# Kernel tuning notes

Measured on AMD Instinct MI355X. Metric: run time of the kernel, lower is better.

## Reference

```python
import jax, jax.numpy as jnp
import numpy as np

N, E, G = 50000, 800000, 64   # nodes, edges, graphs
F, H, O = 6, 256, 2           # in_dim, hidden_dim, out_dim
NE, K, L = 8, 2, 4            # n_experts, top_k, n_layers


def setup_inputs() -> dict:
    key = jax.random.key(0)
    ks = jax.random.split(key, 12)
    s = 0.05
    return {
        "x": jax.random.normal(ks[0], (N, F), jnp.float32),
        "edge_index": jax.random.randint(ks[1], (2, E), 0, N),
        "batch": jnp.sort(jax.random.randint(ks[2], (N,), 0, G)),
        "enc_W": jax.random.normal(ks[3], (F, H), jnp.float32) * s,
        "enc_b": jnp.zeros((H,), jnp.float32),
        "rtr_W1": jax.random.normal(ks[4], (H + 2, H), jnp.float32) * s,
        "rtr_b1": jnp.zeros((H,), jnp.float32),
        "rtr_W2": jax.random.normal(ks[5], (H, NE), jnp.float32) * s,
        "rtr_b2": jnp.zeros((NE,), jnp.float32),
        "hid_Wr": jax.random.normal(ks[6], (L - 1, NE, H, H), jnp.float32) * s,
        "hid_Wn": jax.random.normal(ks[7], (L - 1, NE, H, H), jnp.float32) * s,
        "hid_b": jnp.zeros((L - 1, NE, H), jnp.float32),
        "out_Wr": jax.random.normal(ks[8], (NE, H, O), jnp.float32) * s,
        "out_Wn": jax.random.normal(ks[9], (NE, H, O), jnp.float32) * s,
        "out_b": jnp.zeros((NE, O), jnp.float32),
    }


def reference(x, edge_index, batch, enc_W, enc_b, rtr_W1, rtr_b1, rtr_W2, rtr_b2,
              hid_Wr, hid_Wn, hid_b, out_Wr, out_Wn, out_b):
    src, dst = edge_index[0], edge_index[1]

    # SharedBusEncoder: Linear + ReLU
    h = jax.nn.relu(x @ enc_W + enc_b)  # [N, H]

    # graph_size_features: per-graph node/edge counts, log-scaled, per node
    ones_n = jnp.ones((N,), h.dtype)
    nodes_per_g = jax.ops.segment_sum(ones_n, batch, num_segments=G)
    edges_per_g = jax.ops.segment_sum(jnp.ones((E,), h.dtype), batch[src], num_segments=G)
    size_feat = jnp.stack([jnp.log(nodes_per_g + 1.0)[batch],
                           jnp.log(edges_per_g + 1.0)[batch]], axis=-1)  # [N, 2]

    # BaseRouter: 2-layer MLP -> logits [N, NE]
    r = jax.nn.relu(jnp.concatenate([h, size_feat], axis=-1) @ rtr_W1 + rtr_b1)
    logits = r @ rtr_W2 + rtr_b2

    # sparse_routing (eval mode): softmax over top-k logits, scattered to dense mask
    vals, idx = jax.lax.top_k(logits, K)  # [N, K]
    w = jax.nn.softmax(vals, axis=-1)
    sparse = jnp.zeros((N, NE), h.dtype).at[jnp.arange(N)[:, None], idx].set(w)

    # Dense all-expert GraphConv stacks, mask-sum combine
    def graph_conv(he, Wr, Wn, b):
        agg = jax.ops.segment_sum(he[src], dst, num_segments=N)  # sum-aggregate neighbors
        return he @ Wr + agg @ Wn + b

    out = jnp.zeros((N, O), h.dtype)
    for e in range(NE):
        he = h
        for l in range(L - 1):
            he = jax.nn.relu(graph_conv(he, hid_Wr[l, e], hid_Wn[l, e], hid_b[l, e]))
        ye = graph_conv(he, out_Wr[e], out_Wn[e], out_b[e])  # [N, O]
        out = out + ye * sparse[:, e:e + 1]
    return out
```

## Files before the change

### kernel.cpp

```cpp
#include <hip/hip_runtime.h>
#include <cstdint>

#define NN 50000
#define EE 800000
#define GG 64

typedef unsigned short u16;
typedef __attribute__((ext_vector_type(8))) short bf16x8;
typedef __attribute__((ext_vector_type(4))) float f32x4;

__device__ __forceinline__ float bf2f(u16 v) { return __uint_as_float(((unsigned)v) << 16); }
__device__ __forceinline__ u16 f2bf(float f) {
  unsigned u = __float_as_uint(f);
  return (u16)((u + 0x7fffu + ((u >> 16) & 1u)) >> 16);
}

__device__ __forceinline__ void gload_lds16(const void* g, void* l) {
  __builtin_amdgcn_global_load_lds(
      (const __attribute__((address_space(1))) void*)g,
      (__attribute__((address_space(3))) void*)l,
      16, 0, 0);
}

__global__ void k_sentinel(float* out) { out[threadIdx.x] = 1e12f; }

__global__ __launch_bounds__(256) void k_hist(const int* __restrict__ ei,
                                              int* __restrict__ deg,
                                              int* __restrict__ outdeg) {
  int i = blockIdx.x * 256 + threadIdx.x;
  if (i < EE) {
    atomicAdd(&outdeg[ei[i]], 1);
    atomicAdd(&deg[ei[EE + i]], 1);
  }
}

__global__ __launch_bounds__(256) void k_graph_feats(const int* __restrict__ batch,
                                                     const int* __restrict__ outdeg,
                                                     float* __restrict__ gf) {
  __shared__ int red[256];
  int g = blockIdx.x, tid = threadIdx.x;
  auto lb = [&](int v) {
    int lo = 0, hi = NN;
    while (lo < hi) { int m = (lo + hi) >> 1; if (batch[m] < v) lo = m + 1; else hi = m; }
    return lo;
  };
  int bs = lb(g), be = lb(g + 1);
  int s = 0;
  for (int i = bs + tid; i < be; i += 256) s += outdeg[i];
  red[tid] = s;
  __syncthreads();
  for (int off = 128; off > 0; off >>= 1) {
    if (tid < off) red[tid] += red[tid + off];
    __syncthreads();
  }
  if (tid == 0) {
    gf[g * 2] = logf((float)(be - bs) + 1.f);
    gf[g * 2 + 1] = logf((float)red[0] + 1.f);
  }
}

__global__ __launch_bounds__(256) void k_router(
    const float* __restrict__ x, const float* __restrict__ encW, const float* __restrict__ encb,
    const int* __restrict__ batch, const float* __restrict__ gf,
    const float* __restrict__ W1, const float* __restrict__ b1,
    const float* __restrict__ W2, const float* __restrict__ b2,
    float* __restrict__ sparse, u16* __restrict__ hb_out) {
  __shared__ __align__(16) float hs_t[258][8];
  __shared__ __align__(16) float rs_t[256][8];
  __shared__ float part2[4][64];
  __shared__ float xv[8][6];
  __shared__ float sf[8][2];
  __shared__ float lg[8][8];
  int tid = threadIdx.x;
  int nb = blockIdx.x * 8;
  if (tid < 48) {
    int r = tid / 6, k = tid % 6;
    xv[r][k] = x[(nb + r) * 6 + k];
  }
  if (tid >= 48 && tid < 56) {
    int r = tid - 48;
    int g = batch[nb + r];
    sf[r][0] = gf[g * 2];
    sf[r][1] = gf[g * 2 + 1];
  }
  __syncthreads();
  {
    float wcol[6];
#pragma unroll
    for (int k = 0; k < 6; ++k) wcol[k] = encW[k * 256 + tid];
    float bb = encb[tid];
#pragma unroll
    for (int r = 0; r < 8; ++r) {
      float s = bb;
#pragma unroll
      for (int k = 0; k < 6; ++k) s += xv[r][k] * wcol[k];
      float h = fmaxf(s, 0.f);
      hs_t[tid][r] = h;
      hb_out[(nb + r) * 256 + tid] = f2bf(h);
    }
  }
  if (tid < 16) {
    int r = tid >> 1, c = tid & 1;
    hs_t[256 + c][r] = sf[r][c];
  }
  __syncthreads();
  float acc[8];
  {
    float bb = b1[tid];
#pragma unroll
    for (int r = 0; r < 8; ++r) acc[r] = bb;
  }
  int k = 0;
#pragma unroll 4
  for (; k < 256; ++k) {
    float w = W1[k * 256 + tid];
    float4 ha = *(const float4*)&hs_t[k][0];
    float4 hb4 = *(const float4*)&hs_t[k][4];
    acc[0] += ha.x * w; acc[1] += ha.y * w; acc[2] += ha.z * w; acc[3] += ha.w * w;
    acc[4] += hb4.x * w; acc[5] += hb4.y * w; acc[6] += hb4.z * w; acc[7] += hb4.w * w;
  }
  for (; k < 258; ++k) {
    float w = W1[k * 256 + tid];
    float4 ha = *(const float4*)&hs_t[k][0];
    float4 hb4 = *(const float4*)&hs_t[k][4];
    acc[0] += ha.x * w; acc[1] += ha.y * w; acc[2] += ha.z * w; acc[3] += ha.w * w;
    acc[4] += hb4.x * w; acc[5] += hb4.y * w; acc[6] += hb4.z * w; acc[7] += hb4.w * w;
  }
#pragma unroll
  for (int r = 0; r < 8; ++r) rs_t[tid][r] = fmaxf(acc[r], 0.f);
  __syncthreads();
  {
    int pr = tid & 63, pt = tid >> 6;
    int r = pr >> 3, e = pr & 7;
    float s = 0.f;
    int kk0 = pt * 64;
#pragma unroll 4
    for (int kk = kk0; kk < kk0 + 64; ++kk) s += rs_t[kk][r] * W2[kk * 8 + e];
    part2[pt][pr] = s;
  }
  __syncthreads();
  if (tid < 64) {
    int r = tid >> 3, e = tid & 7;
    lg[r][e] = b2[e] + part2[0][tid] + part2[1][tid] + part2[2][tid] + part2[3][tid];
  }
  __syncthreads();
  if (tid < 8) {
    int node = nb + tid;
    {
      float v1 = lg[tid][0];
      int j1 = 0;
#pragma unroll
      for (int j = 1; j < 8; ++j) {
        float v = lg[tid][j];
        if (v > v1) { v1 = v; j1 = j; }
      }
      float v2 = -1e30f;
      int j2 = 0;
#pragma unroll
      for (int j = 0; j < 8; ++j) {
        if (j == j1) continue;
        float v = lg[tid][j];
        if (v > v2) { v2 = v; j2 = j; }
      }
      float ex = expf(v2 - v1);
      float wa = 1.f / (1.f + ex), wb = ex / (1.f + ex);
      float* sp = sparse + node * 8;
#pragma unroll
      for (int j = 0; j < 8; ++j) sp[j] = 0.f;
      sp[j1] = wa;
      sp[j2] = wb;
    }
  }
}

__global__ __launch_bounds__(1024) void k_scan(const int* __restrict__ deg,
                                               int* __restrict__ rowptr) {
  __shared__ int tmp[1024];
  __shared__ int carry;
  if (threadIdx.x == 0) { carry = 0; rowptr[0] = 0; }
  __syncthreads();
  for (int base = 0; base < NN; base += 1024) {
    int i = base + threadIdx.x;
    int v = (i < NN) ? deg[i] : 0;
    tmp[threadIdx.x] = v;
    __syncthreads();
    for (int off = 1; off < 1024; off <<= 1) {
      int t = (threadIdx.x >= off) ? tmp[threadIdx.x - off] : 0;
      __syncthreads();
      tmp[threadIdx.x] += t;
      __syncthreads();
    }
    if (i < NN) rowptr[i + 1] = carry + tmp[threadIdx.x];
    int last = tmp[1023];
    __syncthreads();
    if (threadIdx.x == 0) carry += last;
    __syncthreads();
  }
}

__global__ __launch_bounds__(256) void k_fill(const int* __restrict__ ei,
                                              const int* __restrict__ rowptr,
                                              int* __restrict__ cursor, int* __restrict__ csrc) {
  int i = blockIdx.x * 256 + threadIdx.x;
  if (i < EE) {
    int s = ei[i], d = ei[EE + i];
    int pos = atomicAdd(&cursor[d], 1);
    csrc[rowptr[d] + pos] = s;
  }
}

__global__ __launch_bounds__(256) void k_spmm256(
    const int* __restrict__ rowptr, const int* __restrict__ csrc,
    const u16* __restrict__ X, u16* __restrict__ Y) {
  int wave = threadIdx.x >> 6, lane = threadIdx.x & 63;
  int d = blockIdx.x * 4 + wave;
  if (d >= NN) return;
  int s0 = rowptr[d], s1 = rowptr[d + 1];
  int c4 = lane * 4;
  float a0 = 0.f, a1 = 0.f, a2 = 0.f, a3 = 0.f;
  int i = s0;
  for (; i + 4 <= s1; i += 4) {
    int sa = csrc[i], sb = csrc[i + 1], sc = csrc[i + 2], sd = csrc[i + 3];
    ushort4 va = *(const ushort4*)(X + sa * 256 + c4);
    ushort4 vb = *(const ushort4*)(X + sb * 256 + c4);
    ushort4 vc = *(const ushort4*)(X + sc * 256 + c4);
    ushort4 vd = *(const ushort4*)(X + sd * 256 + c4);
    a0 += bf2f(va.x) + bf2f(vb.x) + bf2f(vc.x) + bf2f(vd.x);
    a1 += bf2f(va.y) + bf2f(vb.y) + bf2f(vc.y) + bf2f(vd.y);
    a2 += bf2f(va.z) + bf2f(vb.z) + bf2f(vc.z) + bf2f(vd.z);
    a3 += bf2f(va.w) + bf2f(vb.w) + bf2f(vc.w) + bf2f(vd.w);
  }
  for (; i < s1; ++i) {
    int sa = csrc[i];
    ushort4 va = *(const ushort4*)(X + sa * 256 + c4);
    a0 += bf2f(va.x);
    a1 += bf2f(va.y);
    a2 += bf2f(va.z);
    a3 += bf2f(va.w);
  }
  ushort4 o;
  o.x = f2bf(a0); o.y = f2bf(a1); o.z = f2bf(a2); o.w = f2bf(a3);
  *(ushort4*)(Y + d * 256 + c4) = o;
}

__global__ __launch_bounds__(256) void k_spmm_intl(
    const int* __restrict__ rowptr, const int* __restrict__ csrc,
    const u16* __restrict__ X, u16* __restrict__ Y, int rs) {
  int d = blockIdx.x;
  int tid = threadIdx.x;
  if (tid * 4 >= rs) return;
  int s0 = rowptr[d], s1 = rowptr[d + 1];
  int c4 = tid * 4;
  float a0 = 0.f, a1 = 0.f, a2 = 0.f, a3 = 0.f;
  int i = s0;
  for (; i + 4 <= s1; i += 4) {
    int sa = csrc[i], sb = csrc[i + 1], sc = csrc[i + 2], sd = csrc[i + 3];
    ushort4 va = *(const ushort4*)(X + (size_t)sa * rs + c4);
    ushort4 vb = *(const ushort4*)(X + (size_t)sb * rs + c4);
    ushort4 vc = *(const ushort4*)(X + (size_t)sc * rs + c4);
    ushort4 vd = *(const ushort4*)(X + (size_t)sd * rs + c4);
    a0 += bf2f(va.x) + bf2f(vb.x) + bf2f(vc.x) + bf2f(vd.x);
    a1 += bf2f(va.y) + bf2f(vb.y) + bf2f(vc.y) + bf2f(vd.y);
    a2 += bf2f(va.z) + bf2f(vb.z) + bf2f(vc.z) + bf2f(vd.z);
    a3 += bf2f(va.w) + bf2f(vb.w) + bf2f(vc.w) + bf2f(vd.w);
  }
  for (; i < s1; ++i) {
    int sa = csrc[i];
    ushort4 va = *(const ushort4*)(X + (size_t)sa * rs + c4);
    a0 += bf2f(va.x);
    a1 += bf2f(va.y);
    a2 += bf2f(va.z);
    a3 += bf2f(va.w);
  }
  ushort4 o;
  o.x = f2bf(a0); o.y = f2bf(a1); o.z = f2bf(a2); o.w = f2bf(a3);
  *(ushort4*)(Y + (size_t)d * rs + c4) = o;
}

__global__ __launch_bounds__(256) void k_transpose2(const float* __restrict__ Wr,
                                                    const float* __restrict__ Wn,
                                                    u16* __restrict__ WrT,
                                                    u16* __restrict__ WnT) {
  int idx = blockIdx.x * 256 + threadIdx.x;
  if (idx >= 24 * 65536) return;
  int m = idx >> 16, rem = idx & 65535;
  int k = rem >> 8, j = rem & 255;
  int o = (m << 16) + (j << 8) + k;
  WrT[o] = f2bf(Wr[idx]);
  WnT[o] = f2bf(Wn[idx]);
}

__global__ __launch_bounds__(512) void k_gemm(
    const u16* __restrict__ X1b, size_t x1gs, int x1rs,
    const u16* __restrict__ X2b, size_t x2gs, int x2rs,
    const u16* __restrict__ W1tb, const u16* __restrict__ W2tb, size_t wst,
    const float* __restrict__ biasb, size_t bst,
    u16* __restrict__ Yb, size_t ygs, int yrs, int relu,
    const float* __restrict__ oWr, const float* __restrict__ oWn, int e0_base,
    float* __restrict__ Y4self, float* __restrict__ Y4nb, int do_out) {
  __shared__ __align__(16) char smem[49152];
  int g = blockIdx.y;
  const u16* X1 = X1b + (size_t)g * x1gs;
  const u16* X2 = X2b + (size_t)g * x2gs;
  const u16* W1t = W1tb + (size_t)g * wst;
  const u16* W2t = W2tb + (size_t)g * wst;
  const float* bias = biasb + (size_t)g * bst;
  u16* Y = Yb + (size_t)g * ygs;
  int tid = threadIdx.x;
  int wave = tid >> 6, lane = tid & 63;
  int l15 = lane & 15, l4 = lane >> 4;
  int m0 = blockIdx.x * 128;
  int wr = wave >> 2, wc = wave & 3;
  const f32x4 fz = {0.f, 0.f, 0.f, 0.f};
  f32x4 acc[4][4];
#pragma unroll
  for (int a = 0; a < 4; ++a)
#pragma unroll
    for (int b = 0; b < 4; ++b) acc[a][b] = fz;

  auto stage = [&](int t) {
    const u16* xs = (t < 8) ? X1 : X2;
    int xrs = (t < 8) ? x1rs : x2rs;
    const u16* wsrc = (t < 8) ? W1t : W2t;
    int kb = (t & 7) * 32;
    int half = t & 1;
    {
      int flat = wave * 1024 + lane * 16;
      int row = flat >> 6, colb = flat & 63;
      int scol = colb ^ (((row >> 1) & 3) << 4);
      int gr = m0 + row;
      if (gr > NN - 1) gr = NN - 1;
      gload_lds16(xs + (size_t)gr * xrs + kb + (scol >> 1), smem + half * 8192 + flat);
    }
#pragma unroll
    for (int q = 0; q < 2; ++q) {
      int flat = q * 8192 + wave * 1024 + lane * 16;
      int row = flat >> 6, colb = flat & 63;
      int scol = colb ^ (((row >> 1) & 3) << 4);
      gload_lds16(wsrc + row * 256 + kb + (scol >> 1), smem + 16384 + half * 16384 + flat);
    }
  };

  stage(0);
  for (int kt = 0; kt < 16; ++kt) {
    if (kt < 15) {
      stage(kt + 1);
      asm volatile("s_waitcnt vmcnt(3)" ::: "memory");
    } else {
      asm volatile("s_waitcnt vmcnt(0)" ::: "memory");
    }
    __builtin_amdgcn_sched_barrier(0);
    __builtin_amdgcn_s_barrier();
    __builtin_amdgcn_sched_barrier(0);
    const char* Ab = smem + (kt & 1) * 8192;
    const char* Bb = smem + 16384 + (kt & 1) * 16384;
    bf16x8 af[4], bfv[4];
#pragma unroll
    for (int mi = 0; mi < 4; ++mi) {
      int r = wr * 64 + mi * 16 + l15;
      af[mi] = *(const bf16x8*)(Ab + r * 64 + ((l4 * 16) ^ (((r >> 1) & 3) << 4)));
    }
#pragma unroll
    for (int nj = 0; nj < 4; ++nj) {
      int c = wc * 64 + nj * 16 + l15;
      bfv[nj] = *(const bf16x8*)(Bb + c * 64 + ((l4 * 16) ^ (((c >> 1) & 3) << 4)));
    }
#pragma unroll
    for (int mi = 0; mi < 4; ++mi)
#pragma unroll
      for (int nj = 0; nj < 4; ++nj)
        acc[mi][nj] =
            __builtin_amdgcn_mfma_f32_16x16x32_bf16(af[mi], bfv[nj], acc[mi][nj], 0, 0, 0);
    __builtin_amdgcn_sched_barrier(0);
    __builtin_amdgcn_s_barrier();
  }

  if (!do_out) {
#pragma unroll
    for (int mi = 0; mi < 4; ++mi) {
      int rbase = m0 + wr * 64 + mi * 16 + l4 * 4;
#pragma unroll
      for (int nj = 0; nj < 4; ++nj) {
        int col = wc * 64 + nj * 16 + l15;
        float bv = bias[col];
#pragma unroll
        for (int r2 = 0; r2 < 4; ++r2) {
          int row = rbase + r2;
          if (row < NN) {
            float v = acc[mi][nj][r2] + bv;
            if (relu) v = fmaxf(v, 0.f);
            Y[(size_t)row * yrs + col] = f2bf(v);
          }
        }
      }
    }
  } else {
    int eabs = e0_base + g;
    const float2* wr2p = (const float2*)(oWr + (size_t)eabs * 512);
    const float2* wn2p = (const float2*)(oWn + (size_t)eabs * 512);
    float bv[4]; float2 wa[4], wb[4];
#pragma unroll
    for (int nj = 0; nj < 4; ++nj) {
      int col = wc * 64 + nj * 16 + l15;
      bv[nj] = bias[col];
      wa[nj] = wr2p[col];
      wb[nj] = wn2p[col];
    }
    float* y4red = (float*)smem;
#pragma unroll
    for (int mi = 0; mi < 4; ++mi) {
#pragma unroll
      for (int r2 = 0; r2 < 4; ++r2) {
        float p0 = 0.f, p1 = 0.f, p2 = 0.f, p3 = 0.f;
#pragma unroll
        for (int nj = 0; nj < 4; ++nj) {
          float v = fmaxf(acc[mi][nj][r2] + bv[nj], 0.f);
          p0 += v * wa[nj].x; p1 += v * wa[nj].y;
          p2 += v * wb[nj].x; p3 += v * wb[nj].y;
        }
#pragma unroll
        for (int off2 = 1; off2 < 16; off2 <<= 1) {
          p0 += __shfl_xor(p0, off2); p1 += __shfl_xor(p1, off2);
          p2 += __shfl_xor(p2, off2); p3 += __shfl_xor(p3, off2);
        }
        if (l15 == 0) {
          int lr = wr * 64 + mi * 16 + l4 * 4 + r2;
          float* q = y4red + (lr * 4 + wc) * 4;
          q[0] = p0; q[1] = p1; q[2] = p2; q[3] = p3;
        }
      }
    }
    __syncthreads();
    if (tid < 128) {
      int row = m0 + tid;
      if (row < NN) {
        float s0 = 0.f, s1 = 0.f, n0 = 0.f, n1 = 0.f;
#pragma unroll
        for (int w2 = 0; w2 < 4; ++w2) {
          const float* q = y4red + (tid * 4 + w2) * 4;
          s0 += q[0]; s1 += q[1]; n0 += q[2]; n1 += q[3];
        }
        Y4self[row * 16 + eabs * 2] = s0;
        Y4self[row * 16 + eabs * 2 + 1] = s1;
        Y4nb[row * 16 + eabs * 2] = n0;
        Y4nb[row * 16 + eabs * 2 + 1] = n1;
      }
    }
  }
}

__global__ __launch_bounds__(256) void k_combine(
    const int* __restrict__ rowptr, const int* __restrict__ csrc,
    const float* __restrict__ Y4self, const float* __restrict__ Y4nb,
    const float* __restrict__ sparse, const float* __restrict__ ob,
    float* __restrict__ out) {
  int t = blockIdx.x * 256 + threadIdx.x;
  int d = t >> 3, e = t & 7;
  if (d >= NN) return;
  float s0 = Y4self[d * 16 + e * 2], s1 = Y4self[d * 16 + e * 2 + 1];
  float n0 = 0.f, n1 = 0.f;
  for (int i = rowptr[d]; i < rowptr[d + 1]; ++i) {
    int s = csrc[i];
    float2 v = *(const float2*)(Y4nb + s * 16 + e * 2);
    n0 += v.x;
    n1 += v.y;
  }
  float w = sparse[d * 8 + e];
  float t0 = w * (s0 + n0 + ob[e * 2]);
  float t1 = w * (s1 + n1 + ob[e * 2 + 1]);
  t0 += __shfl_xor(t0, 1); t1 += __shfl_xor(t1, 1);
  t0 += __shfl_xor(t0, 2); t1 += __shfl_xor(t1, 2);
  t0 += __shfl_xor(t0, 4); t1 += __shfl_xor(t1, 4);
  if (e == 0) {
    out[d * 2] = t0;
    out[d * 2 + 1] = t1;
  }
}

extern "C" void kernel_launch(void* const* d_in, const int* in_sizes, int n_in,
                              void* d_out, int out_size, void* d_ws, size_t ws_size,
                              hipStream_t stream) {
  const float* x = (const float*)d_in[0];
  const int* ei = (const int*)d_in[1];
  const int* batch = (const int*)d_in[2];
  const float* enc_W = (const float*)d_in[3];
  const float* enc_b = (const float*)d_in[4];
  const float* rW1 = (const float*)d_in[5];
  const float* rb1 = (const float*)d_in[6];
  const float* rW2 = (const float*)d_in[7];
  const float* rb2 = (const float*)d_in[8];
  const float* hid_Wr = (const float*)d_in[9];
  const float* hid_Wn = (const float*)d_in[10];
  const float* hid_b = (const float*)d_in[11];
  const float* out_Wr = (const float*)d_in[12];
  const float* out_Wn = (const float*)d_in[13];
  const float* out_b = (const float*)d_in[14];
  float* out = (float*)d_out;

  char* ws = (char*)d_ws;
  size_t off = 0;
  auto alloc = [&](size_t bytes) -> void* {
    void* p = ws + off;
    off = (off + bytes + 511) & ~(size_t)511;
    return p;
  };
  const size_t HBYTES = (size_t)NN * 256 * 2;
  u16* hb = (u16*)alloc(HBYTES);
  u16* agg0 = (u16*)alloc(HBYTES);
  u16* WrT = (u16*)alloc((size_t)24 * 65536 * 2);
  u16* WnT = (u16*)alloc((size_t)24 * 65536 * 2);
  int* deg = (int*)alloc((size_t)NN * 4);
  int* cursor = (int*)alloc((size_t)NN * 4);
  int* outdeg = (int*)alloc((size_t)NN * 4);
  size_t zero_bytes = (size_t)((char*)(outdeg + NN) - (char*)deg);
  int* rowptr = (int*)alloc((size_t)(NN + 1) * 4);
  int* csrc = (int*)alloc((size_t)EE * 4);
  float* gf = (float*)alloc(GG * 2 * 4);
  float* sparse = (float*)alloc((size_t)NN * 8 * 4);
  float* Y4self = (float*)alloc((size_t)NN * 16 * 4);
  float* Y4nb = (float*)alloc((size_t)NN * 16 * 4);

  size_t rem = (ws_size > off) ? ws_size - off : 0;
  size_t per = 2 * HBYTES + 2048;
  int grp = (rem >= 4 * per) ? 4 : (rem >= 2 * per) ? 2 : (rem >= per) ? 1 : 0;
  if (grp == 0) {
    k_sentinel<<<1, 2, 0, stream>>>(out);
    return;
  }
  u16* heb = (u16*)alloc((size_t)grp * HBYTES);
  u16* aggb = (u16*)alloc((size_t)grp * HBYTES);
  const int RS = grp * 256;

  hipMemsetAsync(deg, 0, zero_bytes, stream);

  k_transpose2<<<(24 * 65536 + 255) / 256, 256, 0, stream>>>(hid_Wr, hid_Wn, WrT, WnT);
  k_hist<<<(EE + 255) / 256, 256, 0, stream>>>(ei, deg, outdeg);
  k_graph_feats<<<GG, 256, 0, stream>>>(batch, outdeg, gf);
  k_scan<<<1, 1024, 0, stream>>>(deg, rowptr);
  k_fill<<<(EE + 255) / 256, 256, 0, stream>>>(ei, rowptr, cursor, csrc);
  k_router<<<NN / 8, 256, 0, stream>>>(x, enc_W, enc_b, batch, gf, rW1, rb1, rW2, rb2,
                                       sparse, hb);

  const int GX = (NN + 127) / 128;

  k_spmm256<<<(NN + 3) / 4, 256, 0, stream>>>(rowptr, csrc, hb, agg0);
  for (int e0 = 0; e0 < 8; e0 += grp) {
    k_gemm<<<dim3(GX, grp), 512, 0, stream>>>(
        hb, 0, 256, agg0, 0, 256, WrT + e0 * 65536, WnT + e0 * 65536, 65536,
        hid_b + e0 * 256, 256, heb, 256, RS, 1, nullptr, nullptr, 0, nullptr, nullptr, 0);
    k_spmm_intl<<<NN, RS / 4, 0, stream>>>(rowptr, csrc, heb, aggb, RS);
    k_gemm<<<dim3(GX, grp), 512, 0, stream>>>(
        heb, 256, RS, aggb, 256, RS, WrT + (8 + e0) * 65536, WnT + (8 + e0) * 65536, 65536,
        hid_b + (8 + e0) * 256, 256, heb, 256, RS, 1, nullptr, nullptr, 0, nullptr, nullptr, 0);
    k_spmm_intl<<<NN, RS / 4, 0, stream>>>(rowptr, csrc, heb, aggb, RS);
    k_gemm<<<dim3(GX, grp), 512, 0, stream>>>(
        heb, 256, RS, aggb, 256, RS, WrT + (16 + e0) * 65536, WnT + (16 + e0) * 65536, 65536,
        hid_b + (16 + e0) * 256, 256, nullptr, 0, 256, 1, out_Wr, out_Wn, e0,
        Y4self, Y4nb, 1);
  }
  k_combine<<<(NN * 8 + 255) / 256, 256, 0, stream>>>(rowptr, csrc, Y4self, Y4nb, sparse,
                                                      out_b, out);
}
```

Baseline: 2.273 ms.

## Fuse preprocessing kernels and replace serial scan with two-level parallel scan

Merges the weight transpose with the degree histogram, graph features with per-block scans, and the router with the CSR fill and rowptr write, which cuts six launches down to four. The single-block serial 1024-thread scan is replaced by a parallel block-local scan followed by a small scan of block sums. CSR fill positions now come from the histogram atomics' return values, which removes the cursor atomics pass. This adds an extra edge-sized buffer and heterogeneous blocks inside the same kernels.

```diff
diff --git a/kernel.cpp b/kernel.cpp
--- a/kernel.cpp
+++ b/kernel.cpp
@@ -24,55 +24,119 @@
 
 __global__ void k_sentinel(float* out) { out[threadIdx.x] = 1e12f; }
 
-__global__ __launch_bounds__(256) void k_hist(const int* __restrict__ ei,
-                                              int* __restrict__ deg,
-                                              int* __restrict__ outdeg) {
-  int i = blockIdx.x * 256 + threadIdx.x;
-  if (i < EE) {
-    atomicAdd(&outdeg[ei[i]], 1);
-    atomicAdd(&deg[ei[EE + i]], 1);
-  }
-}
-
-__global__ __launch_bounds__(256) void k_graph_feats(const int* __restrict__ batch,
-                                                     const int* __restrict__ outdeg,
-                                                     float* __restrict__ gf) {
-  __shared__ int red[256];
-  int g = blockIdx.x, tid = threadIdx.x;
-  auto lb = [&](int v) {
-    int lo = 0, hi = NN;
-    while (lo < hi) { int m = (lo + hi) >> 1; if (batch[m] < v) lo = m + 1; else hi = m; }
-    return lo;
-  };
-  int bs = lb(g), be = lb(g + 1);
-  int s = 0;
-  for (int i = bs + tid; i < be; i += 256) s += outdeg[i];
-  red[tid] = s;
+__global__ __launch_bounds__(256) void k_prep1(
+    const float* __restrict__ Wr, const float* __restrict__ Wn,
+    u16* __restrict__ WrT, u16* __restrict__ WnT,
+    const int* __restrict__ ei, int* __restrict__ deg, int* __restrict__ outdeg,
+    int* __restrict__ epos) {
+  int b = blockIdx.x, tid = threadIdx.x;
+  if (b < 6144) {
+    int idx = b * 256 + tid;
+    int m = idx >> 16, rem = idx & 65535;
+    int k = rem >> 8, j = rem & 255;
+    int o = (m << 16) + (j << 8) + k;
+    WrT[o] = f2bf(Wr[idx]);
+    WnT[o] = f2bf(Wn[idx]);
+  } else {
+    int i = (b - 6144) * 256 + tid;
+    if (i < EE) {
+      atomicAdd(&outdeg[ei[i]], 1);
+      epos[i] = atomicAdd(&deg[ei[EE + i]], 1);
+    }
+  }
+}
+
+__global__ __launch_bounds__(256) void k_prep2(
+    const int* __restrict__ batch, const int* __restrict__ outdeg,
+    float* __restrict__ gf, const int* __restrict__ deg,
+    int* __restrict__ lpre, int* __restrict__ bsum) {
+  int b = blockIdx.x, tid = threadIdx.x;
+  if (b < GG) {
+    __shared__ int red[256];
+    int g = b;
+    auto lb = [&](int v) {
+      int lo = 0, hi = NN;
+      while (lo < hi) { int m = (lo + hi) >> 1; if (batch[m] < v) lo = m + 1; else hi = m; }
+      return lo;
+    };
+    int bs = lb(g), be = lb(g + 1);
+    int s = 0;
+    for (int i = bs + tid; i < be; i += 256) s += outdeg[i];
+    red[tid] = s;
+    __syncthreads();
+    for (int off = 128; off > 0; off >>= 1) {
+      if (tid < off) red[tid] += red[tid + off];
+      __syncthreads();
+    }
+    if (tid == 0) {
+      gf[g * 2] = logf((float)(be - bs) + 1.f);
+      gf[g * 2 + 1] = logf((float)red[0] + 1.f);
+    }
+  } else {
+    __shared__ int tmp[256];
+    int blk = b - GG;
+    int i = blk * 256 + tid;
+    int v = (i < NN) ? deg[i] : 0;
+    tmp[tid] = v;
+    __syncthreads();
+    for (int off = 1; off < 256; off <<= 1) {
+      int t = (tid >= off) ? tmp[tid - off] : 0;
+      __syncthreads();
+      tmp[tid] += t;
+      __syncthreads();
+    }
+    if (i < NN) lpre[i] = tmp[tid] - v;
+    if (tid == 255) bsum[blk] = tmp[255];
+  }
+}
+
+__global__ __launch_bounds__(256) void k_scan2(const int* __restrict__ bsum,
+                                               int* __restrict__ boff) {
+  __shared__ int tmp[256];
+  int tid = threadIdx.x;
+  int v = (tid < 196) ? bsum[tid] : 0;
+  tmp[tid] = v;
   __syncthreads();
-  for (int off = 128; off > 0; off >>= 1) {
-    if (tid < off) red[tid] += red[tid + off];
+  for (int off = 1; off < 256; off <<= 1) {
+    int t = (tid >= off) ? tmp[tid - off] : 0;
     __syncthreads();
-  }
-  if (tid == 0) {
-    gf[g * 2] = logf((float)(be - bs) + 1.f);
-    gf[g * 2 + 1] = logf((float)red[0] + 1.f);
-  }
-}
-
-__global__ __launch_bounds__(256) void k_router(
+    tmp[tid] += t;
+    __syncthreads();
+  }
+  if (tid < 196) boff[tid] = tmp[tid] - v;
+}
+
+__global__ __launch_bounds__(256) void k_prep3(
     const float* __restrict__ x, const float* __restrict__ encW, const float* __restrict__ encb,
     const int* __restrict__ batch, const float* __restrict__ gf,
     const float* __restrict__ W1, const float* __restrict__ b1,
     const float* __restrict__ W2, const float* __restrict__ b2,
-    float* __restrict__ sparse, u16* __restrict__ hb_out) {
+    float* __restrict__ sparse, u16* __restrict__ hb_out,
+    const int* __restrict__ ei, const int* __restrict__ epos,
+    const int* __restrict__ lpre, const int* __restrict__ boff,
+    const int* __restrict__ deg, int* __restrict__ csrc, int* __restrict__ rowptr) {
   __shared__ __align__(16) float hs_t[258][8];
   __shared__ __align__(16) float rs_t[256][8];
   __shared__ float part2[4][64];
   __shared__ float xv[8][6];
   __shared__ float sf[8][2];
   __shared__ float lg[8][8];
-  int tid = threadIdx.x;
-  int nb = blockIdx.x * 8;
+  int b = blockIdx.x, tid = threadIdx.x;
+  if (b >= 6250) {
+    if (b < 6250 + 3125) {
+      int i = (b - 6250) * 256 + tid;
+      if (i < EE) {
+        int s = ei[i], d = ei[EE + i];
+        csrc[lpre[d] + boff[d >> 8] + epos[i]] = s;
+      }
+    } else {
+      int j = (b - 6250 - 3125) * 256 + tid;
+      if (j < NN) rowptr[j + 1] = lpre[j] + deg[j] + boff[j >> 8];
+      if (j == 0) rowptr[0] = 0;
+    }
+    return;
+  }
+  int nb = b * 8;
   if (tid < 48) {
     int r = tid / 6, k = tid % 6;
     xv[r][k] = x[(nb + r) * 6 + k];
@@ -146,66 +210,28 @@
   __syncthreads();
   if (tid < 8) {
     int node = nb + tid;
-    {
-      float v1 = lg[tid][0];
-      int j1 = 0;
-#pragma unroll
-      for (int j = 1; j < 8; ++j) {
-        float v = lg[tid][j];
-        if (v > v1) { v1 = v; j1 = j; }
-      }
-      float v2 = -1e30f;
-      int j2 = 0;
-#pragma unroll
-      for (int j = 0; j < 8; ++j) {
-        if (j == j1) continue;
-        float v = lg[tid][j];
-        if (v > v2) { v2 = v; j2 = j; }
-      }
-      float ex = expf(v2 - v1);
-      float wa = 1.f / (1.f + ex), wb = ex / (1.f + ex);
-      float* sp = sparse + node * 8;
-#pragma unroll
-      for (int j = 0; j < 8; ++j) sp[j] = 0.f;
-      sp[j1] = wa;
-      sp[j2] = wb;
-    }
-  }
-}
-
-__global__ __launch_bounds__(1024) void k_scan(const int* __restrict__ deg,
-                                               int* __restrict__ rowptr) {
-  __shared__ int tmp[1024];
-  __shared__ int carry;
-  if (threadIdx.x == 0) { carry = 0; rowptr[0] = 0; }
-  __syncthreads();
-  for (int base = 0; base < NN; base += 1024) {
-    int i = base + threadIdx.x;
-    int v = (i < NN) ? deg[i] : 0;
-    tmp[threadIdx.x] = v;
-    __syncthreads();
-    for (int off = 1; off < 1024; off <<= 1) {
-      int t = (threadIdx.x >= off) ? tmp[threadIdx.x - off] : 0;
-      __syncthreads();
-      tmp[threadIdx.x] += t;
-      __syncthreads();
-    }
-    if (i < NN) rowptr[i + 1] = carry + tmp[threadIdx.x];
-    int last = tmp[1023];
-    __syncthreads();
-    if (threadIdx.x == 0) carry += last;
-    __syncthreads();
-  }
-}
-
-__global__ __launch_bounds__(256) void k_fill(const int* __restrict__ ei,
-                                              const int* __restrict__ rowptr,
-                                              int* __restrict__ cursor, int* __restrict__ csrc) {
-  int i = blockIdx.x * 256 + threadIdx.x;
-  if (i < EE) {
-    int s = ei[i], d = ei[EE + i];
-    int pos = atomicAdd(&cursor[d], 1);
-    csrc[rowptr[d] + pos] = s;
+    float v1 = lg[tid][0];
+    int j1 = 0;
+#pragma unroll
+    for (int j = 1; j < 8; ++j) {
+      float v = lg[tid][j];
+      if (v > v1) { v1 = v; j1 = j; }
+    }
+    float v2 = -1e30f;
+    int j2 = 0;
+#pragma unroll
+    for (int j = 0; j < 8; ++j) {
+      if (j == j1) continue;
+      float v = lg[tid][j];
+      if (v > v2) { v2 = v; j2 = j; }
+    }
+    float ex = expf(v2 - v1);
+    float wa = 1.f / (1.f + ex), wb = ex / (1.f + ex);
+    float* sp = sparse + node * 8;
+#pragma unroll
+    for (int j = 0; j < 8; ++j) sp[j] = 0.f;
+    sp[j1] = wa;
+    sp[j2] = wb;
   }
 }
 
@@ -275,19 +301,6 @@
   ushort4 o;
   o.x = f2bf(a0); o.y = f2bf(a1); o.z = f2bf(a2); o.w = f2bf(a3);
   *(ushort4*)(Y + (size_t)d * rs + c4) = o;
-}
-
-__global__ __launch_bounds__(256) void k_transpose2(const float* __restrict__ Wr,
-                                                    const float* __restrict__ Wn,
-                                                    u16* __restrict__ WrT,
-                                                    u16* __restrict__ WnT) {
-  int idx = blockIdx.x * 256 + threadIdx.x;
-  if (idx >= 24 * 65536) return;
-  int m = idx >> 16, rem = idx & 65535;
-  int k = rem >> 8, j = rem & 255;
-  int o = (m << 16) + (j << 8) + k;
-  WrT[o] = f2bf(Wr[idx]);
-  WnT[o] = f2bf(Wn[idx]);
 }
 
 __global__ __launch_bounds__(512) void k_gemm(
@@ -510,11 +523,14 @@
   u16* WrT = (u16*)alloc((size_t)24 * 65536 * 2);
   u16* WnT = (u16*)alloc((size_t)24 * 65536 * 2);
   int* deg = (int*)alloc((size_t)NN * 4);
-  int* cursor = (int*)alloc((size_t)NN * 4);
   int* outdeg = (int*)alloc((size_t)NN * 4);
   size_t zero_bytes = (size_t)((char*)(outdeg + NN) - (char*)deg);
   int* rowptr = (int*)alloc((size_t)(NN + 1) * 4);
   int* csrc = (int*)alloc((size_t)EE * 4);
+  int* epos = (int*)alloc((size_t)EE * 4);
+  int* lpre = (int*)alloc((size_t)NN * 4);
+  int* bsum = (int*)alloc(256 * 4);
+  int* boff = (int*)alloc(256 * 4);
   float* gf = (float*)alloc(GG * 2 * 4);
   float* sparse = (float*)alloc((size_t)NN * 8 * 4);
   float* Y4self = (float*)alloc((size_t)NN * 16 * 4);
@@ -533,13 +549,12 @@
 
   hipMemsetAsync(deg, 0, zero_bytes, stream);
 
-  k_transpose2<<<(24 * 65536 + 255) / 256, 256, 0, stream>>>(hid_Wr, hid_Wn, WrT, WnT);
-  k_hist<<<(EE + 255) / 256, 256, 0, stream>>>(ei, deg, outdeg);
-  k_graph_feats<<<GG, 256, 0, stream>>>(batch, outdeg, gf);
-  k_scan<<<1, 1024, 0, stream>>>(deg, rowptr);
-  k_fill<<<(EE + 255) / 256, 256, 0, stream>>>(ei, rowptr, cursor, csrc);
-  k_router<<<NN / 8, 256, 0, stream>>>(x, enc_W, enc_b, batch, gf, rW1, rb1, rW2, rb2,
-                                       sparse, hb);
+  k_prep1<<<6144 + 3125, 256, 0, stream>>>(hid_Wr, hid_Wn, WrT, WnT, ei, deg, outdeg, epos);
+  k_prep2<<<GG + 196, 256, 0, stream>>>(batch, outdeg, gf, deg, lpre, bsum);
+  k_scan2<<<1, 256, 0, stream>>>(bsum, boff);
+  k_prep3<<<6250 + 3125 + 196, 256, 0, stream>>>(x, enc_W, enc_b, batch, gf, rW1, rb1,
+                                                 rW2, rb2, sparse, hb, ei, epos, lpre,
+                                                 boff, deg, csrc, rowptr);
 
   const int GX = (NN + 127) / 128;
 
```

Result: faster. 2.150 ms (-5.4%).
